# Optimization experiments

Measured on AMD Instinct MI355X. Metric: run time of the kernel, lower is better.

Reference implementation:

```python
import jax, jax.numpy as jnp
import numpy as np

U, I, K = 50000, 30000, 64
D0, D1 = 768, 128
N_INTER = 1_000_000
N_LAYERS = 3
BATCH = 4096
EPS = 1e-12


def setup_inputs() -> dict:
    key = jax.random.key(0)
    k1, k2, k3, k4 = jax.random.split(key, 4)
    rng = np.random.default_rng(0)
    # bidirectional bipartite edges: user u <-> item node (U + i)
    u = rng.integers(0, U, size=N_INTER)
    i = rng.integers(0, I, size=N_INTER) + U
    src = np.concatenate([u, i])
    dst = np.concatenate([i, u])
    edge_index = jnp.asarray(np.stack([src, dst]), dtype=jnp.int32)  # [2, 2*N_INTER]
    return {
        "Gu": jax.random.normal(k1, (U, K), dtype=jnp.float32) * 0.1,
        "F0": jax.random.normal(k2, (I, D0), dtype=jnp.float32),
        "F1": jax.random.normal(k3, (I, D1), dtype=jnp.float32),
        "proj_w": jax.random.normal(k4, (D0 + D1, K), dtype=jnp.float32) * 0.03,
        "proj_b": jnp.zeros((K,), dtype=jnp.float32),
        "edge_index": edge_index,
        "user_idx": jnp.asarray(rng.integers(0, U, size=BATCH), dtype=jnp.int32),
        "item_idx": jnp.asarray(rng.integers(0, I, size=BATCH), dtype=jnp.int32),
    }


def _l2_normalize(x):
    # torch.nn.functional.normalize(p=2, dim=1) with eps clamp
    n = jnp.maximum(jnp.linalg.norm(x, axis=1, keepdims=True), EPS)
    return x / n


def reference(Gu, F0, F1, proj_w, proj_b, edge_index, user_idx, item_idx):
    N = U + I
    # concat aggregation: project concatenated multimodal features, L2-normalize rows
    F_proj = _l2_normalize(jnp.concatenate([F0, F1], axis=-1) @ proj_w + proj_b)
    x = jnp.concatenate([Gu, F_proj], axis=0)  # [N, K]

    src, dst = edge_index[0], edge_index[1]
    # gcn_norm without self-loops (LGConv default): D^{-1/2} A D^{-1/2}
    deg = jax.ops.segment_sum(jnp.ones(src.shape[0], dtype=x.dtype), dst, num_segments=N)
    dinv = jnp.where(deg > 0, jax.lax.rsqrt(jnp.maximum(deg, 1.0)), 0.0)
    norm = dinv[src] * dinv[dst]  # [E]

    layers = [x]
    for _ in range(N_LAYERS):
        msg = layers[-1][src] * norm[:, None]  # [E, K]
        layers.append(jax.ops.segment_sum(msg, dst, num_segments=N))

    all_emb = jnp.mean(jnp.stack(layers, axis=0), axis=0)  # layer-wise mean pooling
    gu, fi = all_emb[:U], all_emb[U:]

    # forward(): batched dot product between selected user/item embeddings
    xui = jnp.sum(gu[user_idx] * fi[item_idx], axis=1)  # [BATCH]
    return xui
```

## Files before the change

kernel.cpp:

```cpp
#include <hip/hip_runtime.h>
#include <hip/hip_bf16.h>

#define NU 50000
#define NI 30000
#define NN 80000
#define KDIM 64
#define DD0 768
#define DD1 128
#define DD 896

#define BROWS 128
#define NB (NN / BROWS)
#define CAPB 5120
#define CAP 96
#define REGION_BYTES 24576
#define ENTS_STRIDE (REGION_BYTES / 4)
#define CHUNK_PAIRS 4096

typedef __attribute__((ext_vector_type(8))) short short8v;
typedef __attribute__((ext_vector_type(4))) short short4v;
typedef __attribute__((ext_vector_type(4))) float float4v;
typedef unsigned short ushort_t;

struct bf16pair { short hi, lo; };

__device__ inline bf16pair f32_split_bf16(float v) {
    __hip_bfloat16 h = __float2bfloat16(v);
    float hf = __bfloat162float(h);
    __hip_bfloat16 l = __float2bfloat16(v - hf);
    bf16pair p;
    p.hi = *reinterpret_cast<short*>(&h);
    p.lo = *reinterpret_cast<short*>(&l);
    return p;
}

__device__ inline float bf16bits_to_f32(ushort_t u) {
    return __uint_as_float(((unsigned int)u) << 16);
}

__device__ inline ushort_t f32_to_bf16_rne(float f) {
    unsigned int u = __float_as_uint(f);
    unsigned int r = (u + 0x7FFFu + ((u >> 16) & 1u)) >> 16;
    return (ushort_t)r;
}

__global__ void wtcvt_kernel(const float* __restrict__ W,
                             short* __restrict__ WTh, short* __restrict__ WTl)
{
    const int i = blockIdx.x * 256 + threadIdx.x;
    if (i < DD * KDIM) {
        const int k = i >> 6, col = i & 63;
        const bf16pair p = f32_split_bf16(W[i]);
        WTh[col * DD + k] = p.hi;
        WTl[col * DD + k] = p.lo;
    }
}

__global__ __launch_bounds__(256) void projk_kernel(
    const float* __restrict__ F0, const float* __restrict__ F1,
    const short* __restrict__ WTh, const short* __restrict__ WTl,
    float* __restrict__ Ppart)
{
    __shared__ short Ah[64][72];
    __shared__ short Al[64][72];
    __shared__ short Bh[64][72];
    __shared__ short Bl[64][72];

    const int tid  = threadIdx.x;
    const int wv   = tid >> 6;
    const int lane = tid & 63;
    const int lr   = lane & 15;
    const int grp  = lane >> 4;
    const int rowBase = (blockIdx.x >> 1) * 64;
    const int kz      = blockIdx.x & 1;
    const int cBase   = kz * 7;

    const int aR[4] = { (0*256+tid) >> 4, (1*256+tid) >> 4,
                        (2*256+tid) >> 4, (3*256+tid) >> 4 };
    const int aK    = (tid & 15) * 4;
    const int bCol[2] = { (0*256+tid) >> 3, (1*256+tid) >> 3 };
    const int bK      = (tid & 7) * 8;

    float4   pA[4];
    short8v  pBh[2], pBl[2];

    auto loadChunk = [&](int c) {
        #pragma unroll
        for (int rep = 0; rep < 4; ++rep) {
            const int r = rowBase + aR[rep];
            float4 v = make_float4(0.f, 0.f, 0.f, 0.f);
            if (r < NI) {
                if (c < 12)
                    v = *(const float4*)&F0[(size_t)r * DD0 + c * 64 + aK];
                else
                    v = *(const float4*)&F1[(size_t)r * DD1 + (c - 12) * 64 + aK];
            }
            pA[rep] = v;
        }
        #pragma unroll
        for (int rep = 0; rep < 2; ++rep) {
            pBh[rep] = *(const short8v*)&WTh[(size_t)bCol[rep] * DD + c * 64 + bK];
            pBl[rep] = *(const short8v*)&WTl[(size_t)bCol[rep] * DD + c * 64 + bK];
        }
    };

    float4v acc[4] = {};

    loadChunk(cBase);
    for (int c = 0; c < 7; ++c) {
        #pragma unroll
        for (int rep = 0; rep < 4; ++rep) {
            const float4 v = pA[rep];
            const bf16pair p0 = f32_split_bf16(v.x);
            const bf16pair p1 = f32_split_bf16(v.y);
            const bf16pair p2 = f32_split_bf16(v.z);
            const bf16pair p3 = f32_split_bf16(v.w);
            short4v h4, l4;
            h4[0] = p0.hi; h4[1] = p1.hi; h4[2] = p2.hi; h4[3] = p3.hi;
            l4[0] = p0.lo; l4[1] = p1.lo; l4[2] = p2.lo; l4[3] = p3.lo;
            *(short4v*)&Ah[aR[rep]][aK] = h4;
            *(short4v*)&Al[aR[rep]][aK] = l4;
        }
        #pragma unroll
        for (int rep = 0; rep < 2; ++rep) {
            *(short8v*)&Bh[bCol[rep]][bK] = pBh[rep];
            *(short8v*)&Bl[bCol[rep]][bK] = pBl[rep];
        }
        if (c < 6) loadChunk(cBase + c + 1);
        __syncthreads();

        #pragma unroll
        for (int ks = 0; ks < 2; ++ks) {
            const int ko = ks * 32 + grp * 8;
            const short8v ah = *(const short8v*)&Ah[wv * 16 + lr][ko];
            const short8v al = *(const short8v*)&Al[wv * 16 + lr][ko];
            #pragma unroll
            for (int nt = 0; nt < 4; ++nt) {
                const short8v bh = *(const short8v*)&Bh[nt * 16 + lr][ko];
                const short8v bl = *(const short8v*)&Bl[nt * 16 + lr][ko];
                acc[nt] = __builtin_amdgcn_mfma_f32_16x16x32_bf16(ah, bh, acc[nt], 0, 0, 0);
                acc[nt] = __builtin_amdgcn_mfma_f32_16x16x32_bf16(ah, bl, acc[nt], 0, 0, 0);
                acc[nt] = __builtin_amdgcn_mfma_f32_16x16x32_bf16(al, bh, acc[nt], 0, 0, 0);
            }
        }
        __syncthreads();
    }

    #pragma unroll
    for (int i = 0; i < 4; ++i) {
        const int r = rowBase + wv * 16 + 4 * grp + i;
        if (r < NI) {
            #pragma unroll
            for (int nt = 0; nt < 4; ++nt)
                Ppart[((size_t)kz * NI + r) * KDIM + nt * 16 + lr] = acc[nt][i];
        }
    }
}

__global__ __launch_bounds__(256) void projcomb_kernel(
    const float* __restrict__ Ppart, const float* __restrict__ b,
    const float* __restrict__ dinv,
    float* __restrict__ Fp, ushort_t* __restrict__ curS)
{
    const int wid  = (blockIdx.x * blockDim.x + threadIdx.x) >> 6;
    const int lane = threadIdx.x & 63;
    if (wid >= NI) return;
    const float y = Ppart[(size_t)wid * KDIM + lane]
                  + Ppart[((size_t)NI + wid) * KDIM + lane]
                  + b[lane];
    float ss = y * y;
    ss += __shfl_xor(ss, 1);
    ss += __shfl_xor(ss, 2);
    ss += __shfl_xor(ss, 4);
    ss += __shfl_xor(ss, 8);
    ss += __shfl_xor(ss, 16);
    ss += __shfl_xor(ss, 32);
    const float inv = 1.0f / fmaxf(sqrtf(ss), 1e-12f);
    const float dv  = dinv[NU + wid];
    const float o = y * inv;
    Fp[((size_t)(NU + wid)) * KDIM + lane] = o;
    curS[((size_t)(NU + wid)) * KDIM + lane] = f32_to_bf16_rne(o * dv);
}

__global__ void userinit_kernel(const float* __restrict__ Gu,
                                const float* __restrict__ dinv,
                                ushort_t* __restrict__ curS)
{
    const int i = blockIdx.x * blockDim.x + threadIdx.x;
    if (i < NU * KDIM / 4) {
        const int row = i >> 4;
        const float dv = dinv[row];
        const float4 g = ((const float4*)Gu)[i];
        short4v s;
        s[0] = (short)f32_to_bf16_rne(g.x * dv);
        s[1] = (short)f32_to_bf16_rne(g.y * dv);
        s[2] = (short)f32_to_bf16_rne(g.z * dv);
        s[3] = (short)f32_to_bf16_rne(g.w * dv);
        *(short4v*)&curS[(size_t)i * 4] = s;
    }
}

__global__ __launch_bounds__(256) void part_kernel(
    const int* __restrict__ src, const int* __restrict__ dst,
    int* __restrict__ bcur, unsigned int* __restrict__ ents, int E2)
{
    __shared__ int bcntL[NB];
    __shared__ int bposL[NB];
    const int tid = threadIdx.x;
    const int pairBase = blockIdx.x * CHUNK_PAIRS;

    for (int i = tid; i < NB; i += 256) bcntL[i] = 0;
    __syncthreads();

    #pragma unroll
    for (int it = 0; it < CHUNK_PAIRS / 256; ++it) {
        const int p = pairBase + it * 256 + tid;
        if (p < E2) {
            const int u  = src[p];
            const int iF = dst[p];
            atomicAdd(&bcntL[iF >> 7], 1);
            atomicAdd(&bcntL[u  >> 7], 1);
        }
    }
    __syncthreads();

    for (int bkt = tid; bkt < NB; bkt += 256) {
        const int c = bcntL[bkt];
        bposL[bkt] = (c > 0) ? atomicAdd(&bcur[bkt], c) : 0;
        bcntL[bkt] = 0;
    }
    __syncthreads();

    #pragma unroll
    for (int it = 0; it < CHUNK_PAIRS / 256; ++it) {
        const int p = pairBase + it * 256 + tid;
        if (p < E2) {
            const int u  = src[p];
            const int iF = dst[p];
            {
                const int bkt = iF >> 7;
                const int k = bposL[bkt] + atomicAdd(&bcntL[bkt], 1);
                if (k < CAPB)
                    ents[(size_t)bkt * ENTS_STRIDE + k] =
                        ((unsigned int)(iF & 127) << 16) | (unsigned int)u;
            }
            {
                const int bkt = u >> 7;
                const int k = bposL[bkt] + atomicAdd(&bcntL[bkt], 1);
                if (k < CAPB)
                    ents[(size_t)bkt * ENTS_STRIDE + k] =
                        ((unsigned int)(u & 127) << 16) | (unsigned int)(iF - NU);
            }
        }
    }
}

__global__ __launch_bounds__(256) void toELL_kernel(
    const int* __restrict__ bcur, unsigned int* __restrict__ ents,
    ushort_t* __restrict__ col,
    int* __restrict__ cnt, float* __restrict__ dinv)
{
    __shared__ unsigned int eL[CAPB];
    __shared__ int curL[BROWS];
    const int bkt = blockIdx.x;
    const int tid = threadIdx.x;

    int n = bcur[bkt]; n = (n < CAPB) ? n : CAPB;
    const unsigned int* ep = ents + (size_t)bkt * ENTS_STRIDE;

    for (int j = tid; j < n; j += 256) eL[j] = ep[j];
    if (tid < BROWS) curL[tid] = 0;
    __syncthreads();

    const size_t rowB = (size_t)bkt * BROWS;
    for (int j = tid; j < n; j += 256) {
        const unsigned int e = eL[j];
        const int dl = (int)(e >> 16);
        const int slot = atomicAdd(&curL[dl], 1);
        if (slot < CAP)
            col[(rowB + dl) * CAP + slot] = (ushort_t)(e & 0xFFFFu);
    }
    __syncthreads();

    if (tid < BROWS) {
        int c = curL[tid];
        c = (c < CAP) ? c : CAP;
        const size_t row = rowB + tid;
        cnt[row]  = c;
        dinv[row] = (c > 0) ? rsqrtf((float)c) : 0.0f;
    }
}

__global__ __launch_bounds__(256) void pull_kernel(
    const ushort_t* __restrict__ curS, ushort_t* __restrict__ nxtS,
    const int* __restrict__ cnt,
    const ushort_t* __restrict__ col,
    const float* __restrict__ dinv,
    int rowStart, int nRows)
{
    const int wid = __builtin_amdgcn_readfirstlane(
        (int)((blockIdx.x * blockDim.x + threadIdx.x) >> 6));
    const int lane = threadIdx.x & 63;
    if (wid >= nRows) return;
    const int row = rowStart + wid;

    const unsigned int* cpd = (const unsigned int*)(col + (size_t)row * CAP);
    const int addB = (row < NU) ? NU : 0;
    const int n = cnt[row];

    float a0 = 0.f, a1 = 0.f, a2 = 0.f, a3 = 0.f;
    int j = 0;
    for (; j + 8 <= n; j += 8) {
        const uint4 cc = *(const uint4*)(cpd + (j >> 1));
        const int c0 = (int)(cc.x & 0xFFFFu) + addB;
        const int c1 = (int)(cc.x >> 16)     + addB;
        const int c2 = (int)(cc.y & 0xFFFFu) + addB;
        const int c3 = (int)(cc.y >> 16)     + addB;
        const int c4 = (int)(cc.z & 0xFFFFu) + addB;
        const int c5 = (int)(cc.z >> 16)     + addB;
        const int c6 = (int)(cc.w & 0xFFFFu) + addB;
        const int c7 = (int)(cc.w >> 16)     + addB;
        const float v0 = bf16bits_to_f32(curS[((size_t)c0 << 6) + lane]);
        const float v1 = bf16bits_to_f32(curS[((size_t)c1 << 6) + lane]);
        const float v2 = bf16bits_to_f32(curS[((size_t)c2 << 6) + lane]);
        const float v3 = bf16bits_to_f32(curS[((size_t)c3 << 6) + lane]);
        const float v4 = bf16bits_to_f32(curS[((size_t)c4 << 6) + lane]);
        const float v5 = bf16bits_to_f32(curS[((size_t)c5 << 6) + lane]);
        const float v6 = bf16bits_to_f32(curS[((size_t)c6 << 6) + lane]);
        const float v7 = bf16bits_to_f32(curS[((size_t)c7 << 6) + lane]);
        a0 += v0 + v4; a1 += v1 + v5; a2 += v2 + v6; a3 += v3 + v7;
    }
    for (; j < n; ++j) {
        const unsigned int d = cpd[j >> 1];
        const int c = (int)((j & 1) ? (d >> 16) : (d & 0xFFFFu)) + addB;
        a0 += bf16bits_to_f32(curS[((size_t)c << 6) + lane]);
    }

    const float dv = dinv[row];
    nxtS[((size_t)row << 6) + lane] =
        f32_to_bf16_rne(dv * dv * ((a0 + a1) + (a2 + a3)));
}

__device__ inline float row_acc(int row, float x0, int lane,
                                const ushort_t* __restrict__ S1,
                                const ushort_t* __restrict__ S2,
                                const int* __restrict__ cnt,
                                const ushort_t* __restrict__ col,
                                const float* __restrict__ dinv)
{
    const float dv  = dinv[row];
    const float rdv = (dv > 0.f) ? 1.0f / dv : 0.0f;
    const float s1 = bf16bits_to_f32(S1[((size_t)row << 6) + lane]);
    const float s2 = bf16bits_to_f32(S2[((size_t)row << 6) + lane]);

    const unsigned int* cpd = (const unsigned int*)(col + (size_t)row * CAP);
    const int addB = (row < NU) ? NU : 0;
    const int n = cnt[row];
    float a0 = 0.f, a1 = 0.f, a2 = 0.f, a3 = 0.f;
    int j = 0;
    for (; j + 8 <= n; j += 8) {
        const uint4 cc = *(const uint4*)(cpd + (j >> 1));
        const int c0 = (int)(cc.x & 0xFFFFu) + addB;
        const int c1 = (int)(cc.x >> 16)     + addB;
        const int c2 = (int)(cc.y & 0xFFFFu) + addB;
        const int c3 = (int)(cc.y >> 16)     + addB;
        const int c4 = (int)(cc.z & 0xFFFFu) + addB;
        const int c5 = (int)(cc.z >> 16)     + addB;
        const int c6 = (int)(cc.w & 0xFFFFu) + addB;
        const int c7 = (int)(cc.w >> 16)     + addB;
        const float v0 = bf16bits_to_f32(S2[((size_t)c0 << 6) + lane]);
        const float v1 = bf16bits_to_f32(S2[((size_t)c1 << 6) + lane]);
        const float v2 = bf16bits_to_f32(S2[((size_t)c2 << 6) + lane]);
        const float v3 = bf16bits_to_f32(S2[((size_t)c3 << 6) + lane]);
        const float v4 = bf16bits_to_f32(S2[((size_t)c4 << 6) + lane]);
        const float v5 = bf16bits_to_f32(S2[((size_t)c5 << 6) + lane]);
        const float v6 = bf16bits_to_f32(S2[((size_t)c6 << 6) + lane]);
        const float v7 = bf16bits_to_f32(S2[((size_t)c7 << 6) + lane]);
        a0 += v0 + v4; a1 += v1 + v5; a2 += v2 + v6; a3 += v3 + v7;
    }
    for (; j < n; ++j) {
        const unsigned int d = cpd[j >> 1];
        const int c = (int)((j & 1) ? (d >> 16) : (d & 0xFFFFu)) + addB;
        a0 += bf16bits_to_f32(S2[((size_t)c << 6) + lane]);
    }

    return x0 + (s1 + s2) * rdv + dv * ((a0 + a1) + (a2 + a3));
}

__global__ __launch_bounds__(256) void out_kernel(
    const float* __restrict__ Gu, const float* __restrict__ Fp,
    const ushort_t* __restrict__ S1, const ushort_t* __restrict__ S2,
    const int* __restrict__ cnt, const ushort_t* __restrict__ col,
    const float* __restrict__ dinv,
    const int* __restrict__ uidx, const int* __restrict__ iidx,
    float* __restrict__ out, int B)
{
    const int wid = __builtin_amdgcn_readfirstlane(
        (int)((blockIdx.x * blockDim.x + threadIdx.x) >> 6));
    const int lane = threadIdx.x & 63;
    if (wid >= B) return;
    const int u  = uidx[wid];
    const int rI = NU + iidx[wid];

    const float au = row_acc(u,  Gu[((size_t)u  << 6) + lane], lane,
                             S1, S2, cnt, col, dinv);
    const float ai = row_acc(rI, Fp[((size_t)rI << 6) + lane], lane,
                             S1, S2, cnt, col, dinv);
    float p = au * ai;
    #pragma unroll
    for (int m = 32; m >= 1; m >>= 1) p += __shfl_xor(p, m);
    if (lane == 0) out[wid] = p * (1.0f / 16.0f);
}

extern "C" void kernel_launch(void* const* d_in, const int* in_sizes, int n_in,
                              void* d_out, int out_size, void* d_ws, size_t ws_size,
                              hipStream_t stream)
{
    const float* Gu = (const float*)d_in[0];
    const float* F0 = (const float*)d_in[1];
    const float* F1 = (const float*)d_in[2];
    const float* W  = (const float*)d_in[3];
    const float* pb = (const float*)d_in[4];
    const int* edge = (const int*)d_in[5];
    const int* uidx = (const int*)d_in[6];
    const int* iidx = (const int*)d_in[7];
    const int E  = in_sizes[5] / 2;
    const int E2 = E / 2;
    const int B = in_sizes[6];
    const int* srcp = edge;
    const int* dstp = edge + E;

    const size_t XE = (size_t)NN * KDIM;
    float*    Fp    = (float*)d_ws;
    ushort_t* curA  = (ushort_t*)(Fp + XE);
    ushort_t* curB  = curA + XE;
    float*    dinv  = (float*)(curB + XE);
    int*      cnt   = (int*)(dinv + NN);
    int*      bcur  = cnt + NN;
    short*    WTh   = (short*)(bcur + NB);
    short*    WTl   = WTh + (size_t)KDIM * DD;
    ushort_t* col   = (ushort_t*)(WTl + (size_t)KDIM * DD);
    unsigned int* ents = (unsigned int*)col;
    float*    Ppart = (float*)(col + (size_t)NB * (REGION_BYTES / 2));

    (void)hipMemsetAsync(bcur, 0, NB * sizeof(int), stream);
    part_kernel<<<(E2 + CHUNK_PAIRS - 1) / CHUNK_PAIRS, 256, 0, stream>>>(
        srcp, dstp, bcur, ents, E2);
    toELL_kernel<<<NB, 256, 0, stream>>>(bcur, ents, col, cnt, dinv);

    wtcvt_kernel<<<(DD * KDIM + 255) / 256, 256, 0, stream>>>(W, WTh, WTl);

    projk_kernel<<<((NI + 63) / 64) * 2, 256, 0, stream>>>(F0, F1, WTh, WTl,
                                                           Ppart);
    projcomb_kernel<<<(NI * 64 + 255) / 256, 256, 0, stream>>>(
        Ppart, pb, dinv, Fp, curA);

    userinit_kernel<<<(NU * KDIM / 4 + 255) / 256, 256, 0, stream>>>(
        Gu, dinv, curA);

    const int gridU = (NU * 64 + 255) / 256;
    const int gridI = (NI * 64 + 255) / 256;
    pull_kernel<<<gridU, 256, 0, stream>>>(curA, curB, cnt, col, dinv, 0, NU);
    pull_kernel<<<gridI, 256, 0, stream>>>(curA, curB, cnt, col, dinv, NU, NI);
    pull_kernel<<<gridU, 256, 0, stream>>>(curB, curA, cnt, col, dinv, 0, NU);
    pull_kernel<<<gridI, 256, 0, stream>>>(curB, curA, cnt, col, dinv, NU, NI);

    out_kernel<<<(int)(((size_t)B * 64 + 255) / 256), 256, 0, stream>>>(
        Gu, Fp, curB, curA, cnt, col, dinv, uidx, iidx, (float*)d_out, B);
}
```

Before: 187.3 us.

## Fuse projection split-K halves and normalize epilogue into one kernel

The projection GEMM no longer splits the K dimension across two blocks. Each block now walks all 14 K-chunks and applies bias, L2 normalization, dinv scaling and the bf16 store in its epilogue. This removes the Ppart round-trip through global memory and one kernel launch. In exchange the grid is halved to about 469 blocks, which lowers parallelism on a large GPU and lengthens each block's serial K loop.

```diff
diff --git a/kernel.cpp b/kernel.cpp
--- a/kernel.cpp
+++ b/kernel.cpp
@@ -56,10 +56,11 @@
     }
 }
 
-__global__ __launch_bounds__(256) void projk_kernel(
+__global__ __launch_bounds__(256) void proj_kernel(
     const float* __restrict__ F0, const float* __restrict__ F1,
     const short* __restrict__ WTh, const short* __restrict__ WTl,
-    float* __restrict__ Ppart)
+    const float* __restrict__ b, const float* __restrict__ dinv,
+    float* __restrict__ Fp, ushort_t* __restrict__ curS)
 {
     __shared__ short Ah[64][72];
     __shared__ short Al[64][72];
@@ -71,9 +72,7 @@
     const int lane = tid & 63;
     const int lr   = lane & 15;
     const int grp  = lane >> 4;
-    const int rowBase = (blockIdx.x >> 1) * 64;
-    const int kz      = blockIdx.x & 1;
-    const int cBase   = kz * 7;
+    const int rowBase = blockIdx.x * 64;
 
     const int aR[4] = { (0*256+tid) >> 4, (1*256+tid) >> 4,
                         (2*256+tid) >> 4, (3*256+tid) >> 4 };
@@ -106,8 +105,8 @@
 
     float4v acc[4] = {};
 
-    loadChunk(cBase);
-    for (int c = 0; c < 7; ++c) {
+    loadChunk(0);
+    for (int c = 0; c < 14; ++c) {
         #pragma unroll
         for (int rep = 0; rep < 4; ++rep) {
             const float4 v = pA[rep];
@@ -126,7 +125,7 @@
             *(short8v*)&Bh[bCol[rep]][bK] = pBh[rep];
             *(short8v*)&Bl[bCol[rep]][bK] = pBl[rep];
         }
-        if (c < 6) loadChunk(cBase + c + 1);
+        if (c < 13) loadChunk(c + 1);
         __syncthreads();
 
         #pragma unroll
@@ -146,40 +145,40 @@
         __syncthreads();
     }
 
+    float bias[4];
+    #pragma unroll
+    for (int nt = 0; nt < 4; ++nt) bias[nt] = b[nt * 16 + lr];
+
+    float y[4][4];
+    float ssp[4];
     #pragma unroll
     for (int i = 0; i < 4; ++i) {
+        ssp[i] = 0.f;
+        #pragma unroll
+        for (int nt = 0; nt < 4; ++nt) {
+            y[nt][i] = acc[nt][i] + bias[nt];
+            ssp[i] += y[nt][i] * y[nt][i];
+        }
+    }
+    #pragma unroll
+    for (int i = 0; i < 4; ++i) {
+        float ss = ssp[i];
+        ss += __shfl_xor(ss, 1);
+        ss += __shfl_xor(ss, 2);
+        ss += __shfl_xor(ss, 4);
+        ss += __shfl_xor(ss, 8);
         const int r = rowBase + wv * 16 + 4 * grp + i;
         if (r < NI) {
+            const float inv = 1.0f / fmaxf(sqrtf(ss), 1e-12f);
+            const float dv  = dinv[NU + r];
             #pragma unroll
-            for (int nt = 0; nt < 4; ++nt)
-                Ppart[((size_t)kz * NI + r) * KDIM + nt * 16 + lr] = acc[nt][i];
-        }
-    }
-}
-
-__global__ __launch_bounds__(256) void projcomb_kernel(
-    const float* __restrict__ Ppart, const float* __restrict__ b,
-    const float* __restrict__ dinv,
-    float* __restrict__ Fp, ushort_t* __restrict__ curS)
-{
-    const int wid  = (blockIdx.x * blockDim.x + threadIdx.x) >> 6;
-    const int lane = threadIdx.x & 63;
-    if (wid >= NI) return;
-    const float y = Ppart[(size_t)wid * KDIM + lane]
-                  + Ppart[((size_t)NI + wid) * KDIM + lane]
-                  + b[lane];
-    float ss = y * y;
-    ss += __shfl_xor(ss, 1);
-    ss += __shfl_xor(ss, 2);
-    ss += __shfl_xor(ss, 4);
-    ss += __shfl_xor(ss, 8);
-    ss += __shfl_xor(ss, 16);
-    ss += __shfl_xor(ss, 32);
-    const float inv = 1.0f / fmaxf(sqrtf(ss), 1e-12f);
-    const float dv  = dinv[NU + wid];
-    const float o = y * inv;
-    Fp[((size_t)(NU + wid)) * KDIM + lane] = o;
-    curS[((size_t)(NU + wid)) * KDIM + lane] = f32_to_bf16_rne(o * dv);
+            for (int nt = 0; nt < 4; ++nt) {
+                const float o = y[nt][i] * inv;
+                Fp[(size_t)(NU + r) * KDIM + nt * 16 + lr] = o;
+                curS[(size_t)(NU + r) * KDIM + nt * 16 + lr] = f32_to_bf16_rne(o * dv);
+            }
+        }
+    }
 }
 
 __global__ void userinit_kernel(const float* __restrict__ Gu,
@@ -441,7 +440,6 @@
     short*    WTl   = WTh + (size_t)KDIM * DD;
     ushort_t* col   = (ushort_t*)(WTl + (size_t)KDIM * DD);
     unsigned int* ents = (unsigned int*)col;
-    float*    Ppart = (float*)(col + (size_t)NB * (REGION_BYTES / 2));
 
     (void)hipMemsetAsync(bcur, 0, NB * sizeof(int), stream);
     part_kernel<<<(E2 + CHUNK_PAIRS - 1) / CHUNK_PAIRS, 256, 0, stream>>>(
@@ -450,13 +448,10 @@
 
     wtcvt_kernel<<<(DD * KDIM + 255) / 256, 256, 0, stream>>>(W, WTh, WTl);
 
-    projk_kernel<<<((NI + 63) / 64) * 2, 256, 0, stream>>>(F0, F1, WTh, WTl,
-                                                           Ppart);
-    projcomb_kernel<<<(NI * 64 + 255) / 256, 256, 0, stream>>>(
-        Ppart, pb, dinv, Fp, curA);
-
     userinit_kernel<<<(NU * KDIM / 4 + 255) / 256, 256, 0, stream>>>(
         Gu, dinv, curA);
+    proj_kernel<<<(NI + 63) / 64, 256, 0, stream>>>(F0, F1, WTh, WTl, pb,
+                                                    dinv, Fp, curA);
 
     const int gridU = (NU * 64 + 255) / 256;
     const int gridI = (NI * 64 + 255) / 256;
```

After: 178.3 us. -4.8%, faster.
